# Performance work log

Hardware: AMD Instinct MI355X
Metric: run time of the kernel (lower is better)

Reference implementation:

```python
import jax, jax.numpy as jnp
import numpy as np

T, V, E = 8, 10000, 160000
CIN, H, N, L = 128, 64, 16, 2
COUT = 64
CONV_OUT = 2 * H + 2 * N  # 160
EPS = 1e-5


def setup_inputs() -> dict:
    key = jax.random.key(0)
    ks = jax.random.split(key, 16)
    gn = lambda k, s, sc=1.0: jax.random.normal(k, s, jnp.float32) * sc
    inp = {}
    inp['xs'] = gn(ks[0], (T, V, CIN))
    inp['edge_index'] = jax.random.randint(ks[1], (T, 2, E), 0, V, dtype=jnp.int32)
    inp['Wl0'] = gn(ks[2], (CIN, CONV_OUT), CIN ** -0.5)
    inp['Wr0'] = gn(ks[3], (CIN, CONV_OUT), CIN ** -0.5)
    inp['bc0'] = jnp.zeros((CONV_OUT,), jnp.float32)
    inp['Wl1'] = gn(ks[4], (H, CONV_OUT), H ** -0.5)
    inp['Wr1'] = gn(ks[5], (H, CONV_OUT), H ** -0.5)
    inp['bc1'] = jnp.zeros((CONV_OUT,), jnp.float32)
    inp['Wres0'] = gn(ks[6], (CIN, H), CIN ** -0.5)
    inp['bres0'] = jnp.zeros((H,), jnp.float32)
    inp['Wres1'] = gn(ks[7], (H, H), H ** -0.5)
    inp['bres1'] = jnp.zeros((H,), jnp.float32)
    inp['tk_w'] = gn(ks[8], (H, 3), 3 ** -0.5)
    inp['tk_b'] = jnp.zeros((H,), jnp.float32)
    # hippo init: log_nA = log(arange(1, N+1) + 1), broadcast over layers and d_model
    inp['log_nA'] = jnp.broadcast_to(jnp.log(jnp.arange(1, N + 1, dtype=jnp.float32) + 1.0), (L, H, N)).copy()
    rng = np.random.default_rng(0)
    inp['delta'] = jnp.asarray(np.log(np.exp(rng.uniform(0.001, 0.1, (L, H))) - 1.0), jnp.float32)
    inp['Wmlp'] = gn(ks[9], (H, COUT), H ** -0.5)
    inp['bmlp'] = jnp.zeros((COUT,), jnp.float32)
    return inp


def _ln(x):
    m = x.mean(-1, keepdims=True)
    v = ((x - m) ** 2).mean(-1, keepdims=True)
    return (x - m) * jax.lax.rsqrt(v + EPS)


def _sage(x, ei, Wl, Wr, b):
    # GraphSAGE with mean aggregation: self path + mean over in-neighbors
    src, dst = ei[0], ei[1]
    agg = jax.ops.segment_sum(x[src], dst, num_segments=V)
    cnt = jax.ops.segment_sum(jnp.ones((E,), x.dtype), dst, num_segments=V)
    agg = agg / jnp.maximum(cnt, 1.0)[:, None]
    return x @ Wl + agg @ Wr + b


def _token_mix(x, w, b):
    # depthwise conv1d over time axis (kernel 3, same padding); x: [T, V, H]
    xp = jnp.pad(x, ((1, 1), (0, 0), (0, 0)))
    return xp[:-2] * w[:, 0] + xp[1:-1] * w[:, 1] + xp[2:] * w[:, 2] + b


def _ssm_layer(dts, Bs, Cs, xh, xr, logA, dlt):
    A = -jnp.exp(logA)  # [H, N]

    def step(state, inp):
        dt, B, C, x, r = inp
        dt = jax.nn.softplus(dt + dlt)                 # [V, H]
        A_zoh = jnp.exp(dt[:, :, None] * A)            # [V, H, N]
        state = A_zoh * state + dt[:, :, None] * B[:, None, :] * x[:, :, None]
        y = jax.nn.relu(jnp.einsum('vdn,vn->vd', state, C))
        return state, _ln(y + r)

    state0 = jnp.zeros((V, H, N), dts.dtype)
    _, ys = jax.lax.scan(step, state0, (dts, Bs, Cs, xh, xr))
    return ys  # [T, V, H]


def reference(xs, edge_index, Wl0, Wr0, bc0, Wl1, Wr1, bc1, Wres0, bres0, Wres1, bres1, tk_w, tk_b, log_nA, delta, Wmlp, bmlp):
    convs = [(Wl0, Wr0, bc0), (Wl1, Wr1, bc1)]
    res = [(Wres0, bres0), (Wres1, bres1)]
    for i in range(L):
        Wl, Wr, bc = convs[i]
        Wre, bre = res[i]
        xsr = xs @ Wre + bre                                        # [T, V, H]
        outs = jax.vmap(_sage, in_axes=(0, 0, None, None, None))(xs, edge_index, Wl, Wr, bc)
        xh, dts, Bs, Cs = jnp.split(outs, [H, 2 * H, 2 * H + N], axis=-1)
        xs_ = _token_mix(xh, tk_w, tk_b) if i == 0 else xh
        xs = _ssm_layer(dts, Bs, Cs, xs_, xsr, log_nA[i], delta[i])
    return xs[-1] @ Wmlp + bmlp
```

## Files before the change

kernel.cpp:

```cpp
#include <hip/hip_runtime.h>

#define TT 8
#define VV 10000
#define EE 160000
#define HH 64
#define NN 16
#define CO 64
#define NOUT 224
#define RR (TT * VV)
#define PP 32
#define CHUNK (EE / PP)

typedef float f32x4 __attribute__((ext_vector_type(4)));
typedef float f32x2 __attribute__((ext_vector_type(2)));
typedef __bf16 bf16x8 __attribute__((ext_vector_type(8)));
typedef unsigned int uint;

#define GLOBAL_AS __attribute__((address_space(1)))
#define LDS_AS __attribute__((address_space(3)))

__device__ __forceinline__ unsigned short f2bf(float f) {
  union { float f; unsigned u; } v;
  v.f = f;
  unsigned r = v.u + 0x7fffu + ((v.u >> 16) & 1u);
  return (unsigned short)(r >> 16);
}
__device__ __forceinline__ float bf2f(unsigned h) {
  union { unsigned u; float f; } v;
  v.u = h << 16;
  return v.f;
}
__device__ __forceinline__ f32x2 unpk(uint u) {
  union { uint u; float f; } lo, hi;
  lo.u = u << 16;
  hi.u = u & 0xffff0000u;
  f32x2 r;
  r.x = lo.f;
  r.y = hi.f;
  return r;
}
__device__ __forceinline__ uint pk2(f32x2 v) { return (uint)f2bf(v.x) | ((uint)f2bf(v.y) << 16); }
__device__ __forceinline__ f32x2 red2_1632(f32x2 v) {
  v.x += __shfl_xor(v.x, 16, 64);
  v.y += __shfl_xor(v.y, 16, 64);
  v.x += __shfl_xor(v.x, 32, 64);
  v.y += __shfl_xor(v.y, 32, 64);
  return v;
}

__global__ __launch_bounds__(1024) void hist_part(const int* __restrict__ ei, int* __restrict__ part) {
  __shared__ int cnt[VV];
  const int t = blockIdx.x / PP, p = blockIdx.x % PP;
  const int tid = threadIdx.x;
  for (int i = tid; i < VV; i += 1024) cnt[i] = 0;
  __syncthreads();
  const int* dstp = ei + (long)(t * 2 + 1) * EE + p * CHUNK;
  for (int e = tid; e < CHUNK; e += 1024) atomicAdd(&cnt[dstp[e]], 1);
  __syncthreads();
  int* op = part + (long)blockIdx.x * VV;
  for (int i = tid; i < VV; i += 1024) op[i] = cnt[i];
}

__global__ __launch_bounds__(256) void part_prefix(int* __restrict__ part, int* __restrict__ cnt) {
  int idx = blockIdx.x * 256 + threadIdx.x;
  if (idx >= RR) return;
  int t = idx / VV, v = idx - t * VV;
  long base = ((long)t * PP) * VV + v;
  int x[PP];
#pragma unroll
  for (int p = 0; p < PP; p++) x[p] = part[base + (long)p * VV];
  int s = 0;
#pragma unroll
  for (int p = 0; p < PP; p++) {
    int xx = x[p];
    part[base + (long)p * VV] = s;
    s += xx;
  }
  cnt[idx] = s;
}

__global__ __launch_bounds__(256) void scan_block(const int* __restrict__ cnt, int* __restrict__ off,
                                                  int* __restrict__ bsum) {
  __shared__ int sm[256];
  int i = blockIdx.x * 256 + threadIdx.x;
  int v = (i < RR) ? cnt[i] : 0;
  sm[threadIdx.x] = v;
  __syncthreads();
  for (int d = 1; d < 256; d <<= 1) {
    int t = (threadIdx.x >= d) ? sm[threadIdx.x - d] : 0;
    __syncthreads();
    sm[threadIdx.x] += t;
    __syncthreads();
  }
  if (i < RR) off[i] = sm[threadIdx.x] - v;
  if (threadIdx.x == 255) bsum[blockIdx.x] = sm[255];
}

__global__ __launch_bounds__(512) void scan_tops(int* __restrict__ bsum, int nb) {
  __shared__ int sm[512];
  int v = (threadIdx.x < nb) ? bsum[threadIdx.x] : 0;
  sm[threadIdx.x] = v;
  __syncthreads();
  for (int d = 1; d < 512; d <<= 1) {
    int t = (threadIdx.x >= d) ? sm[threadIdx.x - d] : 0;
    __syncthreads();
    sm[threadIdx.x] += t;
    __syncthreads();
  }
  if (threadIdx.x < nb) bsum[threadIdx.x] = sm[threadIdx.x] - v;
}

__global__ __launch_bounds__(256) void scan_add(int* __restrict__ off, const int* __restrict__ bsum) {
  int i = blockIdx.x * 256 + threadIdx.x;
  if (i < RR) off[i] += bsum[blockIdx.x];
  if (i == 0) off[RR] = TT * EE;
}

__global__ __launch_bounds__(1024) void scatter_part(const int* __restrict__ ei, const int* __restrict__ off,
                                                     const int* __restrict__ part, int* __restrict__ csr) {
  __shared__ int base_s[VV];
  __shared__ int cnt[VV];
  const int t = blockIdx.x / PP, p = blockIdx.x % PP;
  const int tid = threadIdx.x;
  const int* pp = part + (long)blockIdx.x * VV;
  const int* offt = off + t * VV;
  for (int i = tid; i < VV; i += 1024) {
    base_s[i] = offt[i] + pp[i];
    cnt[i] = 0;
  }
  __syncthreads();
  const int* srcp = ei + (long)(t * 2) * EE + p * CHUNK;
  const int* dstp = ei + (long)(t * 2 + 1) * EE + p * CHUNK;
  for (int e = tid; e < CHUNK; e += 1024) {
    int d = dstp[e];
    int r = atomicAdd(&cnt[d], 1);
    csr[base_s[d] + r] = t * VV + srcp[e];
  }
}

__global__ __launch_bounds__(256) void cast_x0(const float* __restrict__ xs, unsigned short* __restrict__ Ahi,
                                               unsigned short* __restrict__ Alo) {
  int idx = blockIdx.x * 256 + threadIdx.x;
  int row = idx >> 5, c4 = (idx & 31) * 4;
  float4 v = *reinterpret_cast<const float4*>(&xs[(long)row * 128 + c4]);
  ushort4 hs, ls;
  hs.x = f2bf(v.x); hs.y = f2bf(v.y); hs.z = f2bf(v.z); hs.w = f2bf(v.w);
  ls.x = f2bf(v.x - bf2f(hs.x)); ls.y = f2bf(v.y - bf2f(hs.y));
  ls.z = f2bf(v.z - bf2f(hs.z)); ls.w = f2bf(v.w - bf2f(hs.w));
  *reinterpret_cast<ushort4*>(&Ahi[(long)row * 256 + c4]) = hs;
  *reinterpret_cast<ushort4*>(&Alo[(long)row * 128 + c4]) = ls;
}

__global__ __launch_bounds__(256) void prep_b(const float* __restrict__ Wl, const float* __restrict__ Wr,
                                              const float* __restrict__ Wres, const float* __restrict__ bc,
                                              const float* __restrict__ bres, int Cin, int Ktot,
                                              unsigned short* __restrict__ Bp, float* __restrict__ bias) {
  int idx = blockIdx.x * 256 + threadIdx.x;
  if (idx >= NOUT * Ktot) return;
  int n = idx / Ktot, k = idx - n * Ktot;
  int reg = k / Cin, kk = k - reg * Cin;
  float w;
  if (reg == 1)
    w = (n < 160) ? Wr[kk * 160 + n] : 0.f;
  else
    w = (n < 160) ? Wl[kk * 160 + n] : Wres[kk * 64 + (n - 160)];
  Bp[idx] = f2bf(w);
  if (k == 0) bias[n] = (n < 160) ? bc[n] : bres[n - 160];
}

__global__ __launch_bounds__(256) void gather0(const int* __restrict__ off, const int* __restrict__ csr,
                                               const uint4* __restrict__ X4, uint4* __restrict__ M4) {
  int sb = (blockIdx.x & 7) * 2500 + (blockIdx.x >> 3);
  int wv = __builtin_amdgcn_readfirstlane(threadIdx.x) >> 6;
  int lane = threadIdx.x & 63;
  int row = sb * 4 + wv;
  int s = off[row], e = off[row + 1];
  int sub = lane >> 4, c = lane & 15;
  f32x2 a0 = {0.f, 0.f}, a1 = a0, a2 = a0, a3 = a0;
  int i = s;
  for (; i + 4 <= e; i += 4) {
    int g = csr[i + sub];
    uint4 w = X4[(long)g * 32 + c];
    a0 += unpk(w.x);
    a1 += unpk(w.y);
    a2 += unpk(w.z);
    a3 += unpk(w.w);
  }
  if (i + sub < e) {
    int g = csr[i + sub];
    uint4 w = X4[(long)g * 32 + c];
    a0 += unpk(w.x);
    a1 += unpk(w.y);
    a2 += unpk(w.z);
    a3 += unpk(w.w);
  }
  a0 = red2_1632(a0);
  a1 = red2_1632(a1);
  a2 = red2_1632(a2);
  a3 = red2_1632(a3);
  if (sub == 0) {
    float inv = 1.f / (float)max(e - s, 1);
    uint4 o;
    o.x = pk2(a0 * inv);
    o.y = pk2(a1 * inv);
    o.z = pk2(a2 * inv);
    o.w = pk2(a3 * inv);
    M4[(long)row * 32 + 16 + c] = o;
  }
}

__global__ __launch_bounds__(256) void gather1(const int* __restrict__ off, const int* __restrict__ csr,
                                               const uint2* __restrict__ X2, uint2* __restrict__ M2) {
  int sb = (blockIdx.x & 7) * 2500 + (blockIdx.x >> 3);
  int wv = __builtin_amdgcn_readfirstlane(threadIdx.x) >> 6;
  int lane = threadIdx.x & 63;
  int row = sb * 4 + wv;
  int s = off[row], e = off[row + 1];
  int sub = lane >> 4, c = lane & 15;
  f32x2 a0 = {0.f, 0.f}, a1 = a0;
  int i = s;
  for (; i + 4 <= e; i += 4) {
    int g = csr[i + sub];
    uint2 w = X2[(long)g * 64 + c];
    a0 += unpk(w.x);
    a1 += unpk(w.y);
  }
  if (i + sub < e) {
    int g = csr[i + sub];
    uint2 w = X2[(long)g * 64 + c];
    a0 += unpk(w.x);
    a1 += unpk(w.y);
  }
  a0 = red2_1632(a0);
  a1 = red2_1632(a1);
  if (sub == 0) {
    float inv = 1.f / (float)max(e - s, 1);
    uint2 o;
    o.x = pk2(a0 * inv);
    o.y = pk2(a1 * inv);
    M2[(long)row * 64 + 16 + c] = o;
  }
}

__device__ __forceinline__ void stage_tile(char* sb, const unsigned short* aptr, long astr,
                                           const unsigned short* Bp, int Ktot, int k0, long row0,
                                           int wid, int lane) {
#pragma unroll
  for (int r = 0; r < 6; ++r) {
    int c = wid * 6 + r;
    const char* gp;
    if (c < 16) {
      int o = c * 1024 + lane * 16;
      int arow = o >> 7;
      int ac16 = (o >> 4) & 7;
      gp = (const char*)aptr + ((row0 + arow) * astr) * 2 + ((ac16 ^ (arow & 7)) << 4);
    } else {
      int o = (c - 16) * 1024 + lane * 16;
      int brow = o >> 7;
      int bc16 = (o >> 4) & 7;
      int browc = brow < NOUT ? brow : (NOUT - 1);
      gp = (const char*)Bp + ((long)browc * Ktot + k0) * 2 + ((bc16 ^ (brow & 7)) << 4);
    }
    __builtin_amdgcn_global_load_lds((const GLOBAL_AS uint*)gp, (LDS_AS uint*)(sb + c * 1024), 16, 0, 0);
  }
}

__global__ __launch_bounds__(512) void gemm_kernel(const unsigned short* __restrict__ Ahi,
                                                   const unsigned short* __restrict__ Alo,
                                                   const unsigned short* __restrict__ Bp,
                                                   const float* __restrict__ bias, float* __restrict__ outs,
                                                   int Ktot, int sw1, int lda, int ldalo) {
  __shared__ char sbuf[2][49152];
  const int tid = threadIdx.x;
  const long row0 = (long)blockIdx.x * 128;
  const int wid = tid >> 6, lane = tid & 63;
  const int wr = wid >> 1, wc = wid & 1;
  const int l15 = lane & 15, lg = lane >> 4;
  f32x4 acc[2][7];
#pragma unroll
  for (int i = 0; i < 2; i++)
#pragma unroll
    for (int n = 0; n < 7; n++) acc[i][n] = (f32x4)(0.f);

  const int nt = Ktot / 64;
  auto asel = [&](int k0, const unsigned short*& aptr, long& astr) {
    if (k0 < sw1) { aptr = Ahi + k0; astr = lda; }
    else { aptr = Alo + (k0 - sw1); astr = ldalo; }
  };
  {
    const unsigned short* aptr; long astr;
    asel(0, aptr, astr);
    stage_tile(sbuf[0], aptr, astr, Bp, Ktot, 0, row0, wid, lane);
  }
  for (int kt = 0; kt < nt; ++kt) {
    const int b = kt & 1;
    if (kt + 1 < nt) {
      const unsigned short* aptr; long astr;
      asel((kt + 1) * 64, aptr, astr);
      stage_tile(sbuf[b ^ 1], aptr, astr, Bp, Ktot, (kt + 1) * 64, row0, wid, lane);
      asm volatile("s_waitcnt vmcnt(6)" ::: "memory");
    } else {
      asm volatile("s_waitcnt vmcnt(0)" ::: "memory");
    }
    __builtin_amdgcn_s_barrier();
    __builtin_amdgcn_sched_barrier(0);
    const char* sb = sbuf[b];
#pragma unroll
    for (int kk = 0; kk < 2; ++kk) {
      const int cswz = (((kk << 2) | lg) ^ (l15 & 7)) << 4;
      bf16x8 af0 = *reinterpret_cast<const bf16x8*>(sb + (wr * 32 + l15) * 128 + cswz);
      bf16x8 af1 = *reinterpret_cast<const bf16x8*>(sb + (wr * 32 + 16 + l15) * 128 + cswz);
#pragma unroll
      for (int n = 0; n < 7; ++n) {
        bf16x8 bfr = *reinterpret_cast<const bf16x8*>(sb + 16384 + (wc * 112 + n * 16 + l15) * 128 + cswz);
        acc[0][n] = __builtin_amdgcn_mfma_f32_16x16x32_bf16(af0, bfr, acc[0][n], 0, 0, 0);
        acc[1][n] = __builtin_amdgcn_mfma_f32_16x16x32_bf16(af1, bfr, acc[1][n], 0, 0, 0);
      }
    }
    __builtin_amdgcn_sched_barrier(0);
    __builtin_amdgcn_s_barrier();
  }
#pragma unroll
  for (int i = 0; i < 2; i++) {
    long grow = row0 + wr * 32 + i * 16 + lg * 4;
#pragma unroll
    for (int n = 0; n < 7; n++) {
      int gcol = wc * 112 + n * 16 + l15;
      float bv = bias[gcol];
#pragma unroll
      for (int r = 0; r < 4; r++) outs[(grow + r) * NOUT + gcol] = acc[i][n][r] + bv;
    }
  }
}

template <int MODE>
__global__ __launch_bounds__(256, 4) void ssm_kernel(const float* __restrict__ outs, const float* __restrict__ logA,
                                                     const float* __restrict__ dlt, const float* __restrict__ tkw,
                                                     const float* __restrict__ tkb, unsigned short* __restrict__ xhi,
                                                     unsigned short* __restrict__ xlo, const float* __restrict__ Wmlp,
                                                     const float* __restrict__ bmlp, float* __restrict__ out) {
  __shared__ float ylds[4][64];
  int wv = __builtin_amdgcn_readfirstlane(threadIdx.x) >> 6;
  int v = blockIdx.x * 4 + wv;
  int h = threadIdx.x & 63;
  f32x2 a2v[8], sv[8];
#pragma unroll
  for (int p = 0; p < 8; p++) {
    a2v[p].x = -__expf(logA[h * NN + 2 * p]) * 1.44269504f;
    a2v[p].y = -__expf(logA[h * NN + 2 * p + 1]) * 1.44269504f;
    sv[p] = (f32x2){0.f, 0.f};
  }
  float dh = dlt[h];
  float w0 = 0.f, w1 = 0.f, w2 = 0.f, tb = 0.f;
  float xhm = 0.f, xh0 = 0.f;
  if (MODE == 0) {
    w0 = tkw[h * 3 + 0];
    w1 = tkw[h * 3 + 1];
    w2 = tkw[h * 3 + 2];
    tb = tkb[h];
  }
  const float* rp = outs + (long)v * NOUT;
  float dtr_c = rp[HH + h] + dh;
  float xvh_c = rp[h];
  float rres_c = rp[160 + h];
  float4 qb_c[4], qc_c[4];
  {
    const float4* bc4 = reinterpret_cast<const float4*>(rp + 2 * HH);
    qb_c[0] = bc4[0]; qb_c[1] = bc4[1]; qb_c[2] = bc4[2]; qb_c[3] = bc4[3];
    if (MODE == 0) { qc_c[0] = bc4[4]; qc_c[1] = bc4[5]; qc_c[2] = bc4[6]; qc_c[3] = bc4[7]; }
  }
  if (MODE == 0) xh0 = xvh_c;
#pragma unroll
  for (int t = 0; t < TT; t++) {
    const float* rpn = rp + (long)VV * NOUT;
    float dtr_n = 0.f, xvh_n = 0.f, rres_n = 0.f;
    float4 qb_n[4], qc_n[4];
    if (t + 1 < TT) {
      dtr_n = rpn[HH + h] + dh;
      xvh_n = rpn[h];
      rres_n = rpn[160 + h];
      const float4* bc4n = reinterpret_cast<const float4*>(rpn + 2 * HH);
      qb_n[0] = bc4n[0]; qb_n[1] = bc4n[1]; qb_n[2] = bc4n[2]; qb_n[3] = bc4n[3];
      if (MODE == 0) { qc_n[0] = bc4n[4]; qc_n[1] = bc4n[5]; qc_n[2] = bc4n[6]; qc_n[3] = bc4n[7]; }
    }
    float dtr = dtr_c;
    float dt = dtr > 20.f ? dtr : __logf(1.f + __expf(dtr));
    float xv;
    if (MODE == 0) {
      float xh1 = (t + 1 < TT) ? xvh_n : 0.f;
      xv = fmaf(xhm, w0, fmaf(xh0, w1, fmaf(xh1, w2, tb)));
      xhm = xh0;
      xh0 = xh1;
    } else {
      xv = xvh_c;
    }
    f32x2 bbv[8] = {{qb_c[0].x, qb_c[0].y}, {qb_c[0].z, qb_c[0].w}, {qb_c[1].x, qb_c[1].y}, {qb_c[1].z, qb_c[1].w},
                    {qb_c[2].x, qb_c[2].y}, {qb_c[2].z, qb_c[2].w}, {qb_c[3].x, qb_c[3].y}, {qb_c[3].z, qb_c[3].w}};
    float dtxv = dt * xv;
#pragma unroll
    for (int p = 0; p < 8; p++) {
      f32x2 arg = a2v[p] * dt;
      f32x2 e = {exp2f(arg.x), exp2f(arg.y)};
      sv[p] = e * sv[p] + bbv[p] * dtxv;
    }
    const bool needY = (MODE == 0) || (t == TT - 1);
    if (needY) {
      float4 c0, c1, c2, c3;
      if (MODE == 0) {
        c0 = qc_c[0]; c1 = qc_c[1]; c2 = qc_c[2]; c3 = qc_c[3];
      } else {
        const float4* bc4 = reinterpret_cast<const float4*>(rp + 2 * HH);
        c0 = bc4[4]; c1 = bc4[5]; c2 = bc4[6]; c3 = bc4[7];
      }
      f32x2 ccv[8] = {{c0.x, c0.y}, {c0.z, c0.w}, {c1.x, c1.y}, {c1.z, c1.w},
                      {c2.x, c2.y}, {c2.z, c2.w}, {c3.x, c3.y}, {c3.z, c3.w}};
      f32x2 yv = {0.f, 0.f};
#pragma unroll
      for (int p = 0; p < 8; p++) yv += sv[p] * ccv[p];
      float y = fmaxf(yv.x + yv.y, 0.f);
      float z = y + rres_c;
      float s1 = z, s2 = z * z;
#pragma unroll
      for (int m = 32; m > 0; m >>= 1) {
        s1 += __shfl_xor(s1, m, 64);
        s2 += __shfl_xor(s2, m, 64);
      }
      float mu = s1 * (1.f / 64.f);
      float var = fmaf(s2, 1.f / 64.f, -mu * mu);
      float o = (z - mu) * rsqrtf(var + 1e-5f);
      if (MODE == 0) {
        long row = (long)t * VV + v;
        unsigned short hi = f2bf(o);
        xhi[row * 256 + h] = hi;
        xlo[row * 128 + h] = f2bf(o - bf2f(hi));
      } else {
        ylds[wv][h] = o;
      }
    }
    dtr_c = dtr_n;
    xvh_c = xvh_n;
    rres_c = rres_n;
    qb_c[0] = qb_n[0]; qb_c[1] = qb_n[1]; qb_c[2] = qb_n[2]; qb_c[3] = qb_n[3];
    if (MODE == 0) { qc_c[0] = qc_n[0]; qc_c[1] = qc_n[1]; qc_c[2] = qc_n[2]; qc_c[3] = qc_n[3]; }
    rp = rpn;
  }
  if (MODE == 1) {
    __syncthreads();
    float acc = bmlp[h];
#pragma unroll 8
    for (int h2 = 0; h2 < 64; h2++) acc = fmaf(ylds[wv][h2], Wmlp[h2 * CO + h], acc);
    out[(long)v * CO + h] = acc;
  }
}

extern "C" void kernel_launch(void* const* d_in, const int* in_sizes, int n_in, void* d_out, int out_size,
                              void* d_ws, size_t ws_size, hipStream_t stream) {
  const float* xs = (const float*)d_in[0];
  const int* ei = (const int*)d_in[1];
  const float* Wl0 = (const float*)d_in[2];
  const float* Wr0 = (const float*)d_in[3];
  const float* bc0 = (const float*)d_in[4];
  const float* Wl1 = (const float*)d_in[5];
  const float* Wr1 = (const float*)d_in[6];
  const float* bc1 = (const float*)d_in[7];
  const float* Wres0 = (const float*)d_in[8];
  const float* bres0 = (const float*)d_in[9];
  const float* Wres1 = (const float*)d_in[10];
  const float* bres1 = (const float*)d_in[11];
  const float* tkw = (const float*)d_in[12];
  const float* tkb = (const float*)d_in[13];
  const float* logA = (const float*)d_in[14];
  const float* dlt = (const float*)d_in[15];
  const float* Wmlp = (const float*)d_in[16];
  const float* bmlp = (const float*)d_in[17];
  float* out = (float*)d_out;

  float* outs = (float*)d_ws;
  unsigned short* Ahi = (unsigned short*)(outs + (long)RR * NOUT);
  unsigned short* Alo = Ahi + (long)RR * 256;
  unsigned short* Bp0 = Alo + (long)RR * 128;
  unsigned short* Bp1 = Bp0 + 224 * 384;
  float* bias0 = (float*)(Bp1 + 224 * 192);
  float* bias1 = bias0 + 224;
  int* off = (int*)(bias1 + 224);
  int* csr = off + RR + 1;
  int* cnt = csr + TT * EE;
  int* bsum = cnt + RR;
  int* part = (int*)outs;

  const int NB = (RR + 255) / 256;

  hist_part<<<TT * PP, 1024, 0, stream>>>(ei, part);
  part_prefix<<<NB, 256, 0, stream>>>(part, cnt);
  scan_block<<<NB, 256, 0, stream>>>(cnt, off, bsum);
  scan_tops<<<1, 512, 0, stream>>>(bsum, NB);
  scan_add<<<NB, 256, 0, stream>>>(off, bsum);
  scatter_part<<<TT * PP, 1024, 0, stream>>>(ei, off, part, csr);

  prep_b<<<(NOUT * 384 + 255) / 256, 256, 0, stream>>>(Wl0, Wr0, Wres0, bc0, bres0, 128, 384, Bp0, bias0);
  prep_b<<<(NOUT * 192 + 255) / 256, 256, 0, stream>>>(Wl1, Wr1, Wres1, bc1, bres1, 64, 192, Bp1, bias1);

  cast_x0<<<RR * 32 / 256, 256, 0, stream>>>(xs, Ahi, Alo);
  gather0<<<RR / 4, 256, 0, stream>>>(off, csr, (const uint4*)Ahi, (uint4*)Ahi);
  gemm_kernel<<<RR / 128, 512, 0, stream>>>(Ahi, Alo, Bp0, bias0, outs, 384, 256, 256, 128);
  ssm_kernel<0><<<VV / 4, 256, 0, stream>>>(outs, logA, dlt, tkw, tkb, Ahi, Alo, nullptr, nullptr, nullptr);

  gather1<<<RR / 4, 256, 0, stream>>>(off, csr, (const uint2*)Ahi, (uint2*)Ahi);
  gemm_kernel<<<RR / 128, 512, 0, stream>>>(Ahi, Alo, Bp1, bias1, outs, 192, 128, 256, 128);
  ssm_kernel<1><<<VV / 4, 256, 0, stream>>>(outs, logA + HH * NN, dlt + HH, nullptr, nullptr, nullptr, nullptr,
                                            Wmlp, bmlp, out);
}
```

Measured before the change: 239.8 us.

## Halve GEMM row tile to 64 and unroll neighbor gather by two

The GEMM block now covers 64 rows instead of 128. Each wave computes one 16-row MFMA strip, so the LDS footprint and accumulator registers shrink and twice as many blocks are launched for better occupancy and load balance across CUs. B-tile staging is redistributed over five interleaved loads per thread, with the last chunk index clamped, and the waitcnt is adjusted to match. Separately, both gather kernels add an 8-edge unrolled loop that issues two independent row loads per iteration to raise memory-level parallelism. The trade-off is that each block reloads the B matrix for half as many rows, which doubles B traffic relative to A.

```diff
diff --git a/kernel.cpp b/kernel.cpp
--- a/kernel.cpp
+++ b/kernel.cpp
@@ -178,6 +178,16 @@
   int sub = lane >> 4, c = lane & 15;
   f32x2 a0 = {0.f, 0.f}, a1 = a0, a2 = a0, a3 = a0;
   int i = s;
+  for (; i + 8 <= e; i += 8) {
+    int g0 = csr[i + sub];
+    int g1 = csr[i + 4 + sub];
+    uint4 w0 = X4[(long)g0 * 32 + c];
+    uint4 w1 = X4[(long)g1 * 32 + c];
+    a0 += unpk(w0.x) + unpk(w1.x);
+    a1 += unpk(w0.y) + unpk(w1.y);
+    a2 += unpk(w0.z) + unpk(w1.z);
+    a3 += unpk(w0.w) + unpk(w1.w);
+  }
   for (; i + 4 <= e; i += 4) {
     int g = csr[i + sub];
     uint4 w = X4[(long)g * 32 + c];
@@ -219,6 +229,14 @@
   int sub = lane >> 4, c = lane & 15;
   f32x2 a0 = {0.f, 0.f}, a1 = a0;
   int i = s;
+  for (; i + 8 <= e; i += 8) {
+    int g0 = csr[i + sub];
+    int g1 = csr[i + 4 + sub];
+    uint2 w0 = X2[(long)g0 * 64 + c];
+    uint2 w1 = X2[(long)g1 * 64 + c];
+    a0 += unpk(w0.x) + unpk(w1.x);
+    a1 += unpk(w0.y) + unpk(w1.y);
+  }
   for (; i + 4 <= e; i += 4) {
     int g = csr[i + sub];
     uint2 w = X2[(long)g * 64 + c];
@@ -246,20 +264,20 @@
                                            const unsigned short* Bp, int Ktot, int k0, long row0,
                                            int wid, int lane) {
 #pragma unroll
-  for (int r = 0; r < 6; ++r) {
-    int c = wid * 6 + r;
+  for (int r = 0; r < 5; ++r) {
+    int c = wid + r * 8;
+    if (c > 35) c = 35;
     const char* gp;
-    if (c < 16) {
+    if (c < 8) {
       int o = c * 1024 + lane * 16;
       int arow = o >> 7;
       int ac16 = (o >> 4) & 7;
       gp = (const char*)aptr + ((row0 + arow) * astr) * 2 + ((ac16 ^ (arow & 7)) << 4);
     } else {
-      int o = (c - 16) * 1024 + lane * 16;
+      int o = (c - 8) * 1024 + lane * 16;
       int brow = o >> 7;
       int bc16 = (o >> 4) & 7;
-      int browc = brow < NOUT ? brow : (NOUT - 1);
-      gp = (const char*)Bp + ((long)browc * Ktot + k0) * 2 + ((bc16 ^ (brow & 7)) << 4);
+      gp = (const char*)Bp + ((long)brow * Ktot + k0) * 2 + ((bc16 ^ (brow & 7)) << 4);
     }
     __builtin_amdgcn_global_load_lds((const GLOBAL_AS uint*)gp, (LDS_AS uint*)(sb + c * 1024), 16, 0, 0);
   }
@@ -270,17 +288,15 @@
                                                    const unsigned short* __restrict__ Bp,
                                                    const float* __restrict__ bias, float* __restrict__ outs,
                                                    int Ktot, int sw1, int lda, int ldalo) {
-  __shared__ char sbuf[2][49152];
+  __shared__ char sbuf[2][36864];
   const int tid = threadIdx.x;
-  const long row0 = (long)blockIdx.x * 128;
+  const long row0 = (long)blockIdx.x * 64;
   const int wid = tid >> 6, lane = tid & 63;
   const int wr = wid >> 1, wc = wid & 1;
   const int l15 = lane & 15, lg = lane >> 4;
-  f32x4 acc[2][7];
-#pragma unroll
-  for (int i = 0; i < 2; i++)
-#pragma unroll
-    for (int n = 0; n < 7; n++) acc[i][n] = (f32x4)(0.f);
+  f32x4 acc[7];
+#pragma unroll
+  for (int n = 0; n < 7; n++) acc[n] = (f32x4)(0.f);
 
   const int nt = Ktot / 64;
   auto asel = [&](int k0, const unsigned short*& aptr, long& astr) {
@@ -298,7 +314,7 @@
       const unsigned short* aptr; long astr;
       asel((kt + 1) * 64, aptr, astr);
       stage_tile(sbuf[b ^ 1], aptr, astr, Bp, Ktot, (kt + 1) * 64, row0, wid, lane);
-      asm volatile("s_waitcnt vmcnt(6)" ::: "memory");
+      asm volatile("s_waitcnt vmcnt(5)" ::: "memory");
     } else {
       asm volatile("s_waitcnt vmcnt(0)" ::: "memory");
     }
@@ -308,28 +324,23 @@
 #pragma unroll
     for (int kk = 0; kk < 2; ++kk) {
       const int cswz = (((kk << 2) | lg) ^ (l15 & 7)) << 4;
-      bf16x8 af0 = *reinterpret_cast<const bf16x8*>(sb + (wr * 32 + l15) * 128 + cswz);
-      bf16x8 af1 = *reinterpret_cast<const bf16x8*>(sb + (wr * 32 + 16 + l15) * 128 + cswz);
+      bf16x8 af = *reinterpret_cast<const bf16x8*>(sb + (wr * 16 + l15) * 128 + cswz);
 #pragma unroll
       for (int n = 0; n < 7; ++n) {
-        bf16x8 bfr = *reinterpret_cast<const bf16x8*>(sb + 16384 + (wc * 112 + n * 16 + l15) * 128 + cswz);
-        acc[0][n] = __builtin_amdgcn_mfma_f32_16x16x32_bf16(af0, bfr, acc[0][n], 0, 0, 0);
-        acc[1][n] = __builtin_amdgcn_mfma_f32_16x16x32_bf16(af1, bfr, acc[1][n], 0, 0, 0);
+        bf16x8 bfr = *reinterpret_cast<const bf16x8*>(sb + 8192 + (wc * 112 + n * 16 + l15) * 128 + cswz);
+        acc[n] = __builtin_amdgcn_mfma_f32_16x16x32_bf16(af, bfr, acc[n], 0, 0, 0);
       }
     }
     __builtin_amdgcn_sched_barrier(0);
     __builtin_amdgcn_s_barrier();
   }
-#pragma unroll
-  for (int i = 0; i < 2; i++) {
-    long grow = row0 + wr * 32 + i * 16 + lg * 4;
-#pragma unroll
-    for (int n = 0; n < 7; n++) {
-      int gcol = wc * 112 + n * 16 + l15;
-      float bv = bias[gcol];
-#pragma unroll
-      for (int r = 0; r < 4; r++) outs[(grow + r) * NOUT + gcol] = acc[i][n][r] + bv;
-    }
+  long grow = row0 + wr * 16 + lg * 4;
+#pragma unroll
+  for (int n = 0; n < 7; n++) {
+    int gcol = wc * 112 + n * 16 + l15;
+    float bv = bias[gcol];
+#pragma unroll
+    for (int r = 0; r < 4; r++) outs[(grow + r) * NOUT + gcol] = acc[n][r] + bv;
   }
 }
 
@@ -502,11 +513,11 @@
 
   cast_x0<<<RR * 32 / 256, 256, 0, stream>>>(xs, Ahi, Alo);
   gather0<<<RR / 4, 256, 0, stream>>>(off, csr, (const uint4*)Ahi, (uint4*)Ahi);
-  gemm_kernel<<<RR / 128, 512, 0, stream>>>(Ahi, Alo, Bp0, bias0, outs, 384, 256, 256, 128);
+  gemm_kernel<<<RR / 64, 512, 0, stream>>>(Ahi, Alo, Bp0, bias0, outs, 384, 256, 256, 128);
   ssm_kernel<0><<<VV / 4, 256, 0, stream>>>(outs, logA, dlt, tkw, tkb, Ahi, Alo, nullptr, nullptr, nullptr);
 
   gather1<<<RR / 4, 256, 0, stream>>>(off, csr, (const uint2*)Ahi, (uint2*)Ahi);
-  gemm_kernel<<<RR / 128, 512, 0, stream>>>(Ahi, Alo, Bp1, bias1, outs, 192, 128, 256, 128);
+  gemm_kernel<<<RR / 64, 512, 0, stream>>>(Ahi, Alo, Bp1, bias1, outs, 192, 128, 256, 128);
   ssm_kernel<1><<<VV / 4, 256, 0, stream>>>(outs, logA + HH * NN, dlt + HH, nullptr, nullptr, nullptr, nullptr,
                                             Wmlp, bmlp, out);
 }
```

After: 230.1 us. 4.0% less time.
